# Performance work log

Measured on AMD Instinct MI355X. Metric: run time of the kernel, lower is better.

Reference implementation:

```python
import jax, jax.numpy as jnp
import numpy as np

NUM_HEADS = 16
EMBED_DIM = 1024
HEAD_DIM = EMBED_DIM // NUM_HEADS  # 64


def setup_inputs() -> dict:
    key = jax.random.key(0)
    k1, k2, k3 = jax.random.split(key, 3)
    x = jax.random.normal(k1, (2, 2048, EMBED_DIM), dtype=jnp.float32)
    # torch Linear(head_dim, 3*head_dim): weight [3*hd, hd], bias [3*hd]
    # stored here as W_qkv [hd, 3*hd] so that y = x @ W_qkv + b
    lim = 1.0 / np.sqrt(HEAD_DIM)
    W_qkv = jax.random.uniform(k2, (HEAD_DIM, 3 * HEAD_DIM), minval=-lim, maxval=lim, dtype=jnp.float32)
    b_qkv = jax.random.uniform(k3, (3 * HEAD_DIM,), minval=-lim, maxval=lim, dtype=jnp.float32)
    return {"x": x, "W_qkv": W_qkv, "b_qkv": b_qkv}


def reference(x, W_qkv, b_qkv):
    B, T, E = x.shape
    # [B, T, E] -> [B, H, T, hd]
    xh = x.reshape(B, T, NUM_HEADS, HEAD_DIM).transpose(0, 2, 1, 3)
    qkv = xh @ W_qkv + b_qkv  # [B, H, T, 3*hd], shared weights across heads
    q, k, v = jnp.split(qkv, 3, axis=-1)
    scale = 1.0 / jnp.sqrt(jnp.asarray(HEAD_DIM, dtype=x.dtype))
    scores = jnp.einsum('bhqd,bhkd->bhqk', q, k) * scale  # [B, H, T, T]
    attn = jax.nn.softmax(scores, axis=-1)
    out = jnp.einsum('bhqk,bhkd->bhqd', attn, v)  # [B, H, T, hd]
    return out.transpose(0, 2, 1, 3).reshape(B, T, E)
```

## Files before the change

kernel.cpp:

```cpp
#include <hip/hip_runtime.h>
#include <hip/hip_bf16.h>

#define T_SEQ   2048
#define EMBED   1024
#define HD      64
#define NHEADS  16
#define NBH     32
#define QSCALE  0.18033688011112042f

typedef __attribute__((ext_vector_type(8))) short short8;
typedef __attribute__((ext_vector_type(4))) float f32x4;
typedef __attribute__((ext_vector_type(2))) unsigned int uint2v;
typedef __attribute__((ext_vector_type(4))) unsigned int uint4v;

#if __has_builtin(__builtin_amdgcn_exp2f)
#define EXP2F __builtin_amdgcn_exp2f
#else
#define EXP2F exp2f
#endif

__device__ __forceinline__ ushort bf16r(float f) {
  union { float f; unsigned u; } v; v.f = f;
  return (ushort)((v.u + 0x8000u) >> 16);
}

__device__ __forceinline__ unsigned pk2bf_perm(float a, float b) {
  union { float f; unsigned u; } ua, ub; ua.f = a; ub.f = b;
  return __builtin_amdgcn_perm(ub.u + 0x8000u, ua.u + 0x8000u, 0x07060302u);
}
#if __has_builtin(__builtin_amdgcn_cvt_pk_bf16_f32)
typedef __attribute__((ext_vector_type(2))) __bf16 bf16x2;
__device__ __forceinline__ unsigned pkbf(float a, float b) {
  union { bf16x2 v; unsigned u; } c;
  c.v = __builtin_amdgcn_cvt_pk_bf16_f32(a, b);
  return c.u;
}
#else
#define pkbf pk2bf_perm
#endif

__device__ __forceinline__ uint2v pl32swap(unsigned a, unsigned b) {
#if __has_builtin(__builtin_amdgcn_permlane32_swap)
  return __builtin_amdgcn_permlane32_swap(a, b, false, false);
#else
  asm("v_permlane32_swap_b32 %0, %1" : "+v"(a), "+v"(b));
  return (uint2v){a, b};
#endif
}
__device__ __forceinline__ uint2v pl16swap(unsigned a, unsigned b) {
#if __has_builtin(__builtin_amdgcn_permlane16_swap)
  return __builtin_amdgcn_permlane16_swap(a, b, false, false);
#else
  asm("v_permlane16_swap_b32 %0, %1" : "+v"(a), "+v"(b));
  return (uint2v){a, b};
#endif
}

__device__ __forceinline__ void async16(const ushort* g, ushort* l) {
  __builtin_amdgcn_global_load_lds(
      (const __attribute__((address_space(1))) unsigned int*)g,
      (__attribute__((address_space(3))) unsigned int*)l, 16, 0, 0);
}

__global__ __launch_bounds__(256) void prep_w(const float* __restrict__ W,
                                              ushort* __restrict__ Wg) {
  const int i = blockIdx.x * 256 + threadIdx.x;
  const int d = i / 192, c = i - d * 192;
  const int phys = c * 64 + (((d >> 3) ^ (c & 7)) << 3) + (d & 7);
  Wg[phys] = bf16r(W[i]);
}

__global__ __launch_bounds__(256) void qkv_proj(
    const float* __restrict__ x, const ushort* __restrict__ Wg,
    const float* __restrict__ bias,
    ushort* __restrict__ Qws, ushort* __restrict__ Kws,
    ushort* __restrict__ Vtws) {
  __shared__ ushort WtL[192 * 64];
  __shared__ __attribute__((aligned(16))) float bl[192];

  const int bx = blockIdx.x;
  const int b  = bx >> 9;
  const int h  = (bx >> 5) & 15;
  const int t0 = (bx & 31) * 64;
  const int tid = threadIdx.x;
  const int wave = tid >> 6, lane = tid & 63;
  const int quad = lane >> 4, n16 = lane & 15;

  const int trow = t0 + wave * 16 + n16;
  const float* xr = x + ((size_t)(b * T_SEQ + trow)) * EMBED + h * HD;
  short8 xa[2];
#pragma unroll
  for (int ks = 0; ks < 2; ks++) {
    f32x4 v0 = *(const f32x4*)(xr + ks * 32 + quad * 8);
    f32x4 v1 = *(const f32x4*)(xr + ks * 32 + quad * 8 + 4);
    short8 f;
    ((unsigned*)&f)[0] = pkbf(v0[0], v0[1]);
    ((unsigned*)&f)[1] = pkbf(v0[2], v0[3]);
    ((unsigned*)&f)[2] = pkbf(v1[0], v1[1]);
    ((unsigned*)&f)[3] = pkbf(v1[2], v1[3]);
    xa[ks] = f;
  }

#pragma unroll
  for (int it = 0; it < 6; it++)
    async16(Wg + it * 2048 + tid * 8, WtL + it * 2048 + wave * 512);
  if (tid < 192) bl[tid] = bias[tid];
  __syncthreads();

  const int bh = b * NHEADS + h;
  const size_t qkbase = (size_t)bh * T_SEQ * HD;
  const int tw = t0 + wave * 16;
  const int sw = n16 & 7;
  const int t = tw + n16;

#pragma unroll
  for (int nt = 0; nt < 12; nt++) {
    const ushort* wrow = WtL + (nt * 16 + n16) * 64;
    const short8 wb0 = *(short8*)(wrow + ((quad ^ sw) << 3));
    const short8 wb1 = *(short8*)(wrow + (((4 | quad) ^ sw) << 3));
    if (nt < 8) {
      f32x4 acc = (f32x4){0.f, 0.f, 0.f, 0.f};
      acc = __builtin_amdgcn_mfma_f32_16x16x32_bf16(wb0, xa[0], acc, 0, 0, 0);
      acc = __builtin_amdgcn_mfma_f32_16x16x32_bf16(wb1, xa[1], acc, 0, 0, 0);
      const f32x4 bv4 = *(const f32x4*)(bl + nt * 16 + quad * 4);
      uint2v pk;
      if (nt < 4) {
        const int d = nt * 16 + quad * 4;
        pk.x = pkbf((acc[0] + bv4[0]) * QSCALE, (acc[1] + bv4[1]) * QSCALE);
        pk.y = pkbf((acc[2] + bv4[2]) * QSCALE, (acc[3] + bv4[3]) * QSCALE);
        *(uint2v*)(Qws + qkbase + (size_t)t * HD + d) = pk;
      } else {
        const int d = (nt - 4) * 16 + quad * 4;
        pk.x = pkbf(acc[0] + bv4[0], acc[1] + bv4[1]);
        pk.y = pkbf(acc[2] + bv4[2], acc[3] + bv4[3]);
        *(uint2v*)(Kws + qkbase + (size_t)t * HD + d) = pk;
      }
    } else {
      f32x4 acc = (f32x4){0.f, 0.f, 0.f, 0.f};
      acc = __builtin_amdgcn_mfma_f32_16x16x32_bf16(xa[0], wb0, acc, 0, 0, 0);
      acc = __builtin_amdgcn_mfma_f32_16x16x32_bf16(xa[1], wb1, acc, 0, 0, 0);
      const float bv = bl[nt * 16 + n16];
      const int d = (nt - 8) * 16 + n16;
      const int tcol = tw + quad * 4;
      uint2v pk;
      pk.x = pkbf(acc[0] + bv, acc[1] + bv);
      pk.y = pkbf(acc[2] + bv, acc[3] + bv);
      *(uint2v*)(Vtws + (size_t)(bh * HD + d) * T_SEQ + tcol) = pk;
    }
  }
}

__global__ __launch_bounds__(256) void flash_attn(
    const ushort* __restrict__ Qws, const ushort* __restrict__ Kws,
    const ushort* __restrict__ Vtws, float* __restrict__ out) {
  __shared__ ushort Ks[4][64 * 64];
  __shared__ ushort Vs[4][64 * 64];

  const int bx = blockIdx.x;
  const int bh = bx & 31;
  const int q0 = (bx >> 5) * 128;
  const int b = bh >> 4, h = bh & 15;
  const int tid = threadIdx.x;
  const int wave = tid >> 6, lane = tid & 63;
  const int quad = lane >> 4, n16 = lane & 15;

  const ushort* Qb = Qws + (size_t)bh * T_SEQ * HD;
  const ushort* Kb = Kws + (size_t)bh * T_SEQ * HD;
  const ushort* Vb = Vtws + (size_t)bh * HD * T_SEQ;

  short8 qa[2][2];
#pragma unroll
  for (int hf = 0; hf < 2; hf++)
#pragma unroll
    for (int ks = 0; ks < 2; ks++) {
      const int row = q0 + wave * 32 + hf * 16 + n16;
      qa[hf][ks] = *(const short8*)(Qb + (size_t)row * HD + ks * 32 + quad * 8);
    }

  const int sr = tid >> 3, sp = tid & 7;
  const int sl = (sp ^ (sr & 7)) * 8;
  const ushort* srcK0 = Kb + (size_t)sr * HD + sl;
  const ushort* srcK1 = Kb + (size_t)(sr + 32) * HD + sl;
  const ushort* srcV0 = Vb + (size_t)sr * T_SEQ + sl;
  const ushort* srcV1 = Vb + (size_t)(sr + 32) * T_SEQ + sl;

  int foff[2];
#pragma unroll
  for (int ks = 0; ks < 2; ks++)
    foff[ks] = n16 * 64 + ((((ks << 2) | quad) ^ (n16 & 7)) << 3);

  short8 ones;
#pragma unroll
  for (int j = 0; j < 8; j++) ones[j] = (short)0x3F80;

  f32x4 o[2][4];
  f32x4 lA[2];
#pragma unroll
  for (int hf = 0; hf < 2; hf++) {
    lA[hf] = (f32x4){0.f, 0.f, 0.f, 0.f};
#pragma unroll
    for (int nt = 0; nt < 4; nt++) o[hf][nt] = (f32x4){0.f, 0.f, 0.f, 0.f};
  }

  auto tile = [&](const ushort* Kt, const ushort* Vt) {
    f32x4 s0[4], s1[4];
    __builtin_amdgcn_s_setprio(1);
#pragma unroll
    for (int nt = 0; nt < 4; nt++) {
      const short8 ka0 = *(short8*)(Kt + (nt << 10) + foff[0]);
      const short8 ka1 = *(short8*)(Kt + (nt << 10) + foff[1]);
      f32x4 a0 = (f32x4){0.f, 0.f, 0.f, 0.f};
      f32x4 a1 = (f32x4){0.f, 0.f, 0.f, 0.f};
      a0 = __builtin_amdgcn_mfma_f32_16x16x32_bf16(ka0, qa[0][0], a0, 0, 0, 0);
      a0 = __builtin_amdgcn_mfma_f32_16x16x32_bf16(ka1, qa[0][1], a0, 0, 0, 0);
      a1 = __builtin_amdgcn_mfma_f32_16x16x32_bf16(ka0, qa[1][0], a1, 0, 0, 0);
      a1 = __builtin_amdgcn_mfma_f32_16x16x32_bf16(ka1, qa[1][1], a1, 0, 0, 0);
      s0[nt] = a0;
      s1[nt] = a1;
    }
    __builtin_amdgcn_s_setprio(0);

    short8 pa[2][2];
#pragma unroll
    for (int hf = 0; hf < 2; hf++) {
      unsigned P01[4], P23[4];
#pragma unroll
      for (int nt = 0; nt < 4; nt++) {
        const f32x4 sv = hf ? s1[nt] : s0[nt];
        float p0 = EXP2F(sv[0]), p1 = EXP2F(sv[1]);
        float p2 = EXP2F(sv[2]), p3 = EXP2F(sv[3]);
        P01[nt] = pkbf(p0, p1);
        P23[nt] = pkbf(p2, p3);
      }
#pragma unroll
      for (int ks = 0; ks < 2; ks++) {
        uint2v tA = pl32swap(P01[2 * ks], P01[2 * ks + 1]);
        uint2v uA = pl16swap(tA.x, tA.y);
        uint2v tB = pl32swap(P23[2 * ks], P23[2 * ks + 1]);
        uint2v uB = pl16swap(tB.x, tB.y);
        union { uint4v u; short8 s; } c;
        c.u = (uint4v){uA.x, uB.x, uA.y, uB.y};
        pa[hf][ks] = c.s;
      }
    }

    __builtin_amdgcn_s_setprio(1);
#pragma unroll
    for (int nt = 0; nt < 4; nt++) {
      const short8 vb0 = *(short8*)(Vt + (nt << 10) + foff[0]);
      const short8 vb1 = *(short8*)(Vt + (nt << 10) + foff[1]);
      o[0][nt] = __builtin_amdgcn_mfma_f32_16x16x32_bf16(pa[0][0], vb0, o[0][nt], 0, 0, 0);
      o[0][nt] = __builtin_amdgcn_mfma_f32_16x16x32_bf16(pa[0][1], vb1, o[0][nt], 0, 0, 0);
      o[1][nt] = __builtin_amdgcn_mfma_f32_16x16x32_bf16(pa[1][0], vb0, o[1][nt], 0, 0, 0);
      o[1][nt] = __builtin_amdgcn_mfma_f32_16x16x32_bf16(pa[1][1], vb1, o[1][nt], 0, 0, 0);
    }
#pragma unroll
    for (int hf = 0; hf < 2; hf++) {
      lA[hf] = __builtin_amdgcn_mfma_f32_16x16x32_bf16(pa[hf][0], ones, lA[hf], 0, 0, 0);
      lA[hf] = __builtin_amdgcn_mfma_f32_16x16x32_bf16(pa[hf][1], ones, lA[hf], 0, 0, 0);
    }
    __builtin_amdgcn_s_setprio(0);
  };

  async16(srcK0, Ks[0] + wave * 512);
  async16(srcK1, Ks[0] + 2048 + wave * 512);
  async16(srcV0, Vs[0] + wave * 512);
  async16(srcV1, Vs[0] + 2048 + wave * 512);
  async16(srcK0 + 64 * HD, Ks[1] + wave * 512);
  async16(srcK1 + 64 * HD, Ks[1] + 2048 + wave * 512);
  async16(srcV0 + 64, Vs[1] + wave * 512);
  async16(srcV1 + 64, Vs[1] + 2048 + wave * 512);
  srcK0 += 128 * HD; srcK1 += 128 * HD; srcV0 += 128; srcV1 += 128;

  for (int j = 0; j < 16; j++) {
    __builtin_amdgcn_sched_barrier(0);
    asm volatile("s_waitcnt vmcnt(0)" ::: "memory");
    __builtin_amdgcn_s_barrier();
    __builtin_amdgcn_sched_barrier(0);
    const int b0 = (j & 1) << 1;
    if (j < 15) {
      async16(srcK0, Ks[b0 ^ 2] + wave * 512);
      async16(srcK1, Ks[b0 ^ 2] + 2048 + wave * 512);
      async16(srcV0, Vs[b0 ^ 2] + wave * 512);
      async16(srcV1, Vs[b0 ^ 2] + 2048 + wave * 512);
      async16(srcK0 + 64 * HD, Ks[(b0 ^ 2) | 1] + wave * 512);
      async16(srcK1 + 64 * HD, Ks[(b0 ^ 2) | 1] + 2048 + wave * 512);
      async16(srcV0 + 64, Vs[(b0 ^ 2) | 1] + wave * 512);
      async16(srcV1 + 64, Vs[(b0 ^ 2) | 1] + 2048 + wave * 512);
      srcK0 += 128 * HD; srcK1 += 128 * HD; srcV0 += 128; srcV1 += 128;
    }
    tile(Ks[b0], Vs[b0]);
    tile(Ks[b0 | 1], Vs[b0 | 1]);
  }

#pragma unroll
  for (int hf = 0; hf < 2; hf++) {
#pragma unroll
    for (int r = 0; r < 4; r++) {
      const float rl = 1.0f / lA[hf][r];
      const int row = q0 + wave * 32 + hf * 16 + quad * 4 + r;
#pragma unroll
      for (int nt = 0; nt < 4; nt++) {
        const int d = nt * 16 + n16;
        out[(size_t)(b * T_SEQ + row) * EMBED + h * HD + d] = o[hf][nt][r] * rl;
      }
    }
  }
}

extern "C" void kernel_launch(void* const* d_in, const int* in_sizes, int n_in,
                              void* d_out, int out_size, void* d_ws, size_t ws_size,
                              hipStream_t stream) {
  (void)in_sizes; (void)n_in; (void)out_size; (void)ws_size;
  const float* x    = (const float*)d_in[0];
  const float* W    = (const float*)d_in[1];
  const float* bias = (const float*)d_in[2];
  float* out = (float*)d_out;

  const size_t elems = (size_t)NBH * T_SEQ * HD;
  ushort* Qws  = (ushort*)d_ws;
  ushort* Kws  = Qws + elems;
  ushort* Vtws = Kws + elems;
  ushort* Wg   = Vtws + elems;

  prep_w<<<dim3(48), dim3(256), 0, stream>>>(W, Wg);
  qkv_proj<<<dim3(1024), dim3(256), 0, stream>>>(x, Wg, bias, Qws, Kws, Vtws);
  flash_attn<<<dim3(512), dim3(256), 0, stream>>>(Qws, Kws, Vtws, out);
}
```

Before: 128.7 us.

## Fuse weight prep into projection and deepen K/V prefetch pipeline

Drops the separate prep_w kernel launch. Each projection block now loads the fp32 weights itself, converts them to bf16 and writes them into the swizzled LDS layout. The attention loop goes from paired 128-row tiles with a full vmcnt(0) drain to single 64-row tiles over a 4-slot ring. It prefetches two tiles ahead and uses partial vmcnt waits, so K/V loads overlap compute better. In exchange every projection block redoes the weight conversion, and the attention loop runs twice as many barriers.

```diff
diff --git a/kernel.cpp b/kernel.cpp
--- a/kernel.cpp
+++ b/kernel.cpp
@@ -62,16 +62,8 @@
       (__attribute__((address_space(3))) unsigned int*)l, 16, 0, 0);
 }
 
-__global__ __launch_bounds__(256) void prep_w(const float* __restrict__ W,
-                                              ushort* __restrict__ Wg) {
-  const int i = blockIdx.x * 256 + threadIdx.x;
-  const int d = i / 192, c = i - d * 192;
-  const int phys = c * 64 + (((d >> 3) ^ (c & 7)) << 3) + (d & 7);
-  Wg[phys] = bf16r(W[i]);
-}
-
 __global__ __launch_bounds__(256) void qkv_proj(
-    const float* __restrict__ x, const ushort* __restrict__ Wg,
+    const float* __restrict__ x, const float* __restrict__ W,
     const float* __restrict__ bias,
     ushort* __restrict__ Qws, ushort* __restrict__ Kws,
     ushort* __restrict__ Vtws) {
@@ -102,8 +94,18 @@
   }
 
 #pragma unroll
-  for (int it = 0; it < 6; it++)
-    async16(Wg + it * 2048 + tid * 8, WtL + it * 2048 + wave * 512);
+  for (int k = 0; k < 12; k++) {
+    const int i4 = k * 256 + tid;
+    const f32x4 w4 = *(const f32x4*)(W + (size_t)i4 * 4);
+    const int i = i4 * 4;
+    const int d = i / 192;
+    const int c0 = i - d * 192;
+#pragma unroll
+    for (int j = 0; j < 4; j++) {
+      const int c = c0 + j;
+      WtL[c * 64 + (((d >> 3) ^ (c & 7)) << 3) + (d & 7)] = bf16r(w4[j]);
+    }
+  }
   if (tid < 192) bl[tid] = bias[tid];
   __syncthreads();
 
@@ -179,10 +181,10 @@
 
   const int sr = tid >> 3, sp = tid & 7;
   const int sl = (sp ^ (sr & 7)) * 8;
-  const ushort* srcK0 = Kb + (size_t)sr * HD + sl;
-  const ushort* srcK1 = Kb + (size_t)(sr + 32) * HD + sl;
-  const ushort* srcV0 = Vb + (size_t)sr * T_SEQ + sl;
-  const ushort* srcV1 = Vb + (size_t)(sr + 32) * T_SEQ + sl;
+  const ushort* pK0 = Kb + (size_t)sr * HD + sl;
+  const ushort* pK1 = Kb + (size_t)(sr + 32) * HD + sl;
+  const ushort* pV0 = Vb + (size_t)sr * T_SEQ + sl;
+  const ushort* pV1 = Vb + (size_t)(sr + 32) * T_SEQ + sl;
 
   int foff[2];
 #pragma unroll
@@ -202,7 +204,36 @@
     for (int nt = 0; nt < 4; nt++) o[hf][nt] = (f32x4){0.f, 0.f, 0.f, 0.f};
   }
 
-  auto tile = [&](const ushort* Kt, const ushort* Vt) {
+  async16(pK0, Ks[0] + wave * 512);
+  async16(pK1, Ks[0] + 2048 + wave * 512);
+  async16(pV0, Vs[0] + wave * 512);
+  async16(pV1, Vs[0] + 2048 + wave * 512);
+  async16(pK0 + 64 * HD, Ks[1] + wave * 512);
+  async16(pK1 + 64 * HD, Ks[1] + 2048 + wave * 512);
+  async16(pV0 + 64, Vs[1] + wave * 512);
+  async16(pV1 + 64, Vs[1] + 2048 + wave * 512);
+  pK0 += 128 * HD; pK1 += 128 * HD; pV0 += 128; pV1 += 128;
+
+  for (int kt = 0; kt < 32; kt++) {
+    const int cb = kt & 3;
+    if (kt < 30) {
+      const int pb = (kt + 2) & 3;
+      async16(pK0, Ks[pb] + wave * 512);
+      async16(pK1, Ks[pb] + 2048 + wave * 512);
+      async16(pV0, Vs[pb] + wave * 512);
+      async16(pV1, Vs[pb] + 2048 + wave * 512);
+      pK0 += 64 * HD; pK1 += 64 * HD; pV0 += 64; pV1 += 64;
+    }
+    __builtin_amdgcn_sched_barrier(0);
+    if (kt < 30)       asm volatile("s_waitcnt vmcnt(8)" ::: "memory");
+    else if (kt == 30) asm volatile("s_waitcnt vmcnt(4)" ::: "memory");
+    else               asm volatile("s_waitcnt vmcnt(0)" ::: "memory");
+    __builtin_amdgcn_s_barrier();
+    __builtin_amdgcn_sched_barrier(0);
+
+    const ushort* Kt = Ks[cb];
+    const ushort* Vt = Vs[cb];
+
     f32x4 s0[4], s1[4];
     __builtin_amdgcn_s_setprio(1);
 #pragma unroll
@@ -260,37 +291,6 @@
       lA[hf] = __builtin_amdgcn_mfma_f32_16x16x32_bf16(pa[hf][1], ones, lA[hf], 0, 0, 0);
     }
     __builtin_amdgcn_s_setprio(0);
-  };
-
-  async16(srcK0, Ks[0] + wave * 512);
-  async16(srcK1, Ks[0] + 2048 + wave * 512);
-  async16(srcV0, Vs[0] + wave * 512);
-  async16(srcV1, Vs[0] + 2048 + wave * 512);
-  async16(srcK0 + 64 * HD, Ks[1] + wave * 512);
-  async16(srcK1 + 64 * HD, Ks[1] + 2048 + wave * 512);
-  async16(srcV0 + 64, Vs[1] + wave * 512);
-  async16(srcV1 + 64, Vs[1] + 2048 + wave * 512);
-  srcK0 += 128 * HD; srcK1 += 128 * HD; srcV0 += 128; srcV1 += 128;
-
-  for (int j = 0; j < 16; j++) {
-    __builtin_amdgcn_sched_barrier(0);
-    asm volatile("s_waitcnt vmcnt(0)" ::: "memory");
-    __builtin_amdgcn_s_barrier();
-    __builtin_amdgcn_sched_barrier(0);
-    const int b0 = (j & 1) << 1;
-    if (j < 15) {
-      async16(srcK0, Ks[b0 ^ 2] + wave * 512);
-      async16(srcK1, Ks[b0 ^ 2] + 2048 + wave * 512);
-      async16(srcV0, Vs[b0 ^ 2] + wave * 512);
-      async16(srcV1, Vs[b0 ^ 2] + 2048 + wave * 512);
-      async16(srcK0 + 64 * HD, Ks[(b0 ^ 2) | 1] + wave * 512);
-      async16(srcK1 + 64 * HD, Ks[(b0 ^ 2) | 1] + 2048 + wave * 512);
-      async16(srcV0 + 64, Vs[(b0 ^ 2) | 1] + wave * 512);
-      async16(srcV1 + 64, Vs[(b0 ^ 2) | 1] + 2048 + wave * 512);
-      srcK0 += 128 * HD; srcK1 += 128 * HD; srcV0 += 128; srcV1 += 128;
-    }
-    tile(Ks[b0], Vs[b0]);
-    tile(Ks[b0 | 1], Vs[b0 | 1]);
   }
 
 #pragma unroll
@@ -321,9 +321,7 @@
   ushort* Qws  = (ushort*)d_ws;
   ushort* Kws  = Qws + elems;
   ushort* Vtws = Kws + elems;
-  ushort* Wg   = Vtws + elems;
-
-  prep_w<<<dim3(48), dim3(256), 0, stream>>>(W, Wg);
-  qkv_proj<<<dim3(1024), dim3(256), 0, stream>>>(x, Wg, bias, Qws, Kws, Vtws);
+
+  qkv_proj<<<dim3(1024), dim3(256), 0, stream>>>(x, W, bias, Qws, Kws, Vtws);
   flash_attn<<<dim3(512), dim3(256), 0, stream>>>(Qws, Kws, Vtws, out);
 }
```

New measurement: 128.2 us. About the same (-0.3%).

## Use two waves per attention block with 64 query rows each and deeper K/V pipeline

Applied to the files above, without the earlier changes.

The flash attention kernel now runs 128 threads per block, with each wave handling 64 query rows (four 16-row groups) instead of 32. Each K/V tile loaded from LDS is reused across more queries. The K/V staging becomes a four-slot ring with prefetch two tiles ahead and partial vmcnt waits, replacing the wait-for-all double buffer. The trade is more accumulator registers per wave and fewer waves per block, which may lower occupancy.

```diff
diff --git a/kernel.cpp b/kernel.cpp
--- a/kernel.cpp
+++ b/kernel.cpp
@@ -150,7 +150,7 @@
   }
 }
 
-__global__ __launch_bounds__(256) void flash_attn(
+__global__ __launch_bounds__(128) void flash_attn(
     const ushort* __restrict__ Qws, const ushort* __restrict__ Kws,
     const ushort* __restrict__ Vtws, float* __restrict__ out) {
   __shared__ ushort Ks[4][64 * 64];
@@ -168,21 +168,19 @@
   const ushort* Kb = Kws + (size_t)bh * T_SEQ * HD;
   const ushort* Vb = Vtws + (size_t)bh * HD * T_SEQ;
 
-  short8 qa[2][2];
-#pragma unroll
-  for (int hf = 0; hf < 2; hf++)
+  short8 qa[4][2];
+#pragma unroll
+  for (int qg = 0; qg < 4; qg++)
 #pragma unroll
     for (int ks = 0; ks < 2; ks++) {
-      const int row = q0 + wave * 32 + hf * 16 + n16;
-      qa[hf][ks] = *(const short8*)(Qb + (size_t)row * HD + ks * 32 + quad * 8);
-    }
-
-  const int sr = tid >> 3, sp = tid & 7;
-  const int sl = (sp ^ (sr & 7)) * 8;
-  const ushort* srcK0 = Kb + (size_t)sr * HD + sl;
-  const ushort* srcK1 = Kb + (size_t)(sr + 32) * HD + sl;
-  const ushort* srcV0 = Vb + (size_t)sr * T_SEQ + sl;
-  const ushort* srcV1 = Vb + (size_t)(sr + 32) * T_SEQ + sl;
+      const int row = q0 + wave * 64 + qg * 16 + n16;
+      qa[qg][ks] = *(const short8*)(Qb + (size_t)row * HD + ks * 32 + quad * 8);
+    }
+
+  const int sr8 = lane >> 3, sp = lane & 7;
+  const int sl = (sp ^ sr8) * 8;
+  const ushort* pK = Kb + (size_t)(wave * 32 + sr8) * HD + sl;
+  const ushort* pV = Vb + (size_t)(wave * 32 + sr8) * T_SEQ + sl;
 
   int foff[2];
 #pragma unroll
@@ -193,42 +191,73 @@
 #pragma unroll
   for (int j = 0; j < 8; j++) ones[j] = (short)0x3F80;
 
-  f32x4 o[2][4];
-  f32x4 lA[2];
-#pragma unroll
-  for (int hf = 0; hf < 2; hf++) {
-    lA[hf] = (f32x4){0.f, 0.f, 0.f, 0.f};
-#pragma unroll
-    for (int nt = 0; nt < 4; nt++) o[hf][nt] = (f32x4){0.f, 0.f, 0.f, 0.f};
-  }
-
-  auto tile = [&](const ushort* Kt, const ushort* Vt) {
-    f32x4 s0[4], s1[4];
-    __builtin_amdgcn_s_setprio(1);
+  f32x4 o[4][4];
+  f32x4 lA[4];
+#pragma unroll
+  for (int qg = 0; qg < 4; qg++) {
+    lA[qg] = (f32x4){0.f, 0.f, 0.f, 0.f};
+#pragma unroll
+    for (int nt = 0; nt < 4; nt++) o[qg][nt] = (f32x4){0.f, 0.f, 0.f, 0.f};
+  }
+
+#pragma unroll
+  for (int j = 0; j < 4; j++) {
+    async16(pK + j * 8 * HD, Ks[0] + wave * 2048 + j * 512);
+    async16(pV + j * 8 * T_SEQ, Vs[0] + wave * 2048 + j * 512);
+  }
+#pragma unroll
+  for (int j = 0; j < 4; j++) {
+    async16(pK + 64 * HD + j * 8 * HD, Ks[1] + wave * 2048 + j * 512);
+    async16(pV + 64 + j * 8 * T_SEQ, Vs[1] + wave * 2048 + j * 512);
+  }
+  pK += 128 * HD; pV += 128;
+
+  for (int kt = 0; kt < 32; kt++) {
+    const int cb = kt & 3;
+    if (kt < 30) {
+      const int pb = (kt + 2) & 3;
+#pragma unroll
+      for (int j = 0; j < 4; j++) {
+        async16(pK + j * 8 * HD, Ks[pb] + wave * 2048 + j * 512);
+        async16(pV + j * 8 * T_SEQ, Vs[pb] + wave * 2048 + j * 512);
+      }
+      pK += 64 * HD; pV += 64;
+    }
+    __builtin_amdgcn_sched_barrier(0);
+    if (kt < 30)       asm volatile("s_waitcnt vmcnt(16)" ::: "memory");
+    else if (kt == 30) asm volatile("s_waitcnt vmcnt(8)" ::: "memory");
+    else               asm volatile("s_waitcnt vmcnt(0)" ::: "memory");
+    __builtin_amdgcn_s_barrier();
+    __builtin_amdgcn_sched_barrier(0);
+
+    const ushort* Kt = Ks[cb];
+    const ushort* Vt = Vs[cb];
+
+    short8 ka[4][2];
 #pragma unroll
     for (int nt = 0; nt < 4; nt++) {
-      const short8 ka0 = *(short8*)(Kt + (nt << 10) + foff[0]);
-      const short8 ka1 = *(short8*)(Kt + (nt << 10) + foff[1]);
-      f32x4 a0 = (f32x4){0.f, 0.f, 0.f, 0.f};
-      f32x4 a1 = (f32x4){0.f, 0.f, 0.f, 0.f};
-      a0 = __builtin_amdgcn_mfma_f32_16x16x32_bf16(ka0, qa[0][0], a0, 0, 0, 0);
-      a0 = __builtin_amdgcn_mfma_f32_16x16x32_bf16(ka1, qa[0][1], a0, 0, 0, 0);
-      a1 = __builtin_amdgcn_mfma_f32_16x16x32_bf16(ka0, qa[1][0], a1, 0, 0, 0);
-      a1 = __builtin_amdgcn_mfma_f32_16x16x32_bf16(ka1, qa[1][1], a1, 0, 0, 0);
-      s0[nt] = a0;
-      s1[nt] = a1;
-    }
-    __builtin_amdgcn_s_setprio(0);
-
-    short8 pa[2][2];
-#pragma unroll
-    for (int hf = 0; hf < 2; hf++) {
+      ka[nt][0] = *(short8*)(Kt + (nt << 10) + foff[0]);
+      ka[nt][1] = *(short8*)(Kt + (nt << 10) + foff[1]);
+    }
+
+    short8 pa[4][2];
+#pragma unroll
+    for (int qg = 0; qg < 4; qg++) {
+      f32x4 s[4];
+      __builtin_amdgcn_s_setprio(1);
+#pragma unroll
+      for (int nt = 0; nt < 4; nt++) {
+        f32x4 a = (f32x4){0.f, 0.f, 0.f, 0.f};
+        a = __builtin_amdgcn_mfma_f32_16x16x32_bf16(ka[nt][0], qa[qg][0], a, 0, 0, 0);
+        a = __builtin_amdgcn_mfma_f32_16x16x32_bf16(ka[nt][1], qa[qg][1], a, 0, 0, 0);
+        s[nt] = a;
+      }
+      __builtin_amdgcn_s_setprio(0);
       unsigned P01[4], P23[4];
 #pragma unroll
       for (int nt = 0; nt < 4; nt++) {
-        const f32x4 sv = hf ? s1[nt] : s0[nt];
-        float p0 = EXP2F(sv[0]), p1 = EXP2F(sv[1]);
-        float p2 = EXP2F(sv[2]), p3 = EXP2F(sv[3]);
+        float p0 = EXP2F(s[nt][0]), p1 = EXP2F(s[nt][1]);
+        float p2 = EXP2F(s[nt][2]), p3 = EXP2F(s[nt][3]);
         P01[nt] = pkbf(p0, p1);
         P23[nt] = pkbf(p2, p3);
       }
@@ -240,69 +269,39 @@
         uint2v uB = pl16swap(tB.x, tB.y);
         union { uint4v u; short8 s; } c;
         c.u = (uint4v){uA.x, uB.x, uA.y, uB.y};
-        pa[hf][ks] = c.s;
+        pa[qg][ks] = c.s;
       }
     }
 
     __builtin_amdgcn_s_setprio(1);
+#pragma unroll
+    for (int qg = 0; qg < 4; qg++) {
+      lA[qg] = __builtin_amdgcn_mfma_f32_16x16x32_bf16(pa[qg][0], ones, lA[qg], 0, 0, 0);
+      lA[qg] = __builtin_amdgcn_mfma_f32_16x16x32_bf16(pa[qg][1], ones, lA[qg], 0, 0, 0);
+    }
 #pragma unroll
     for (int nt = 0; nt < 4; nt++) {
       const short8 vb0 = *(short8*)(Vt + (nt << 10) + foff[0]);
       const short8 vb1 = *(short8*)(Vt + (nt << 10) + foff[1]);
-      o[0][nt] = __builtin_amdgcn_mfma_f32_16x16x32_bf16(pa[0][0], vb0, o[0][nt], 0, 0, 0);
-      o[0][nt] = __builtin_amdgcn_mfma_f32_16x16x32_bf16(pa[0][1], vb1, o[0][nt], 0, 0, 0);
-      o[1][nt] = __builtin_amdgcn_mfma_f32_16x16x32_bf16(pa[1][0], vb0, o[1][nt], 0, 0, 0);
-      o[1][nt] = __builtin_amdgcn_mfma_f32_16x16x32_bf16(pa[1][1], vb1, o[1][nt], 0, 0, 0);
-    }
-#pragma unroll
-    for (int hf = 0; hf < 2; hf++) {
-      lA[hf] = __builtin_amdgcn_mfma_f32_16x16x32_bf16(pa[hf][0], ones, lA[hf], 0, 0, 0);
-      lA[hf] = __builtin_amdgcn_mfma_f32_16x16x32_bf16(pa[hf][1], ones, lA[hf], 0, 0, 0);
+#pragma unroll
+      for (int qg = 0; qg < 4; qg++) {
+        o[qg][nt] = __builtin_amdgcn_mfma_f32_16x16x32_bf16(pa[qg][0], vb0, o[qg][nt], 0, 0, 0);
+        o[qg][nt] = __builtin_amdgcn_mfma_f32_16x16x32_bf16(pa[qg][1], vb1, o[qg][nt], 0, 0, 0);
+      }
     }
     __builtin_amdgcn_s_setprio(0);
-  };
-
-  async16(srcK0, Ks[0] + wave * 512);
-  async16(srcK1, Ks[0] + 2048 + wave * 512);
-  async16(srcV0, Vs[0] + wave * 512);
-  async16(srcV1, Vs[0] + 2048 + wave * 512);
-  async16(srcK0 + 64 * HD, Ks[1] + wave * 512);
-  async16(srcK1 + 64 * HD, Ks[1] + 2048 + wave * 512);
-  async16(srcV0 + 64, Vs[1] + wave * 512);
-  async16(srcV1 + 64, Vs[1] + 2048 + wave * 512);
-  srcK0 += 128 * HD; srcK1 += 128 * HD; srcV0 += 128; srcV1 += 128;
-
-  for (int j = 0; j < 16; j++) {
-    __builtin_amdgcn_sched_barrier(0);
-    asm volatile("s_waitcnt vmcnt(0)" ::: "memory");
-    __builtin_amdgcn_s_barrier();
-    __builtin_amdgcn_sched_barrier(0);
-    const int b0 = (j & 1) << 1;
-    if (j < 15) {
-      async16(srcK0, Ks[b0 ^ 2] + wave * 512);
-      async16(srcK1, Ks[b0 ^ 2] + 2048 + wave * 512);
-      async16(srcV0, Vs[b0 ^ 2] + wave * 512);
-      async16(srcV1, Vs[b0 ^ 2] + 2048 + wave * 512);
-      async16(srcK0 + 64 * HD, Ks[(b0 ^ 2) | 1] + wave * 512);
-      async16(srcK1 + 64 * HD, Ks[(b0 ^ 2) | 1] + 2048 + wave * 512);
-      async16(srcV0 + 64, Vs[(b0 ^ 2) | 1] + wave * 512);
-      async16(srcV1 + 64, Vs[(b0 ^ 2) | 1] + 2048 + wave * 512);
-      srcK0 += 128 * HD; srcK1 += 128 * HD; srcV0 += 128; srcV1 += 128;
-    }
-    tile(Ks[b0], Vs[b0]);
-    tile(Ks[b0 | 1], Vs[b0 | 1]);
-  }
-
-#pragma unroll
-  for (int hf = 0; hf < 2; hf++) {
+  }
+
+#pragma unroll
+  for (int qg = 0; qg < 4; qg++) {
 #pragma unroll
     for (int r = 0; r < 4; r++) {
-      const float rl = 1.0f / lA[hf][r];
-      const int row = q0 + wave * 32 + hf * 16 + quad * 4 + r;
+      const float rl = 1.0f / lA[qg][r];
+      const int row = q0 + wave * 64 + qg * 16 + quad * 4 + r;
 #pragma unroll
       for (int nt = 0; nt < 4; nt++) {
         const int d = nt * 16 + n16;
-        out[(size_t)(b * T_SEQ + row) * EMBED + h * HD + d] = o[hf][nt][r] * rl;
+        out[(size_t)(b * T_SEQ + row) * EMBED + h * HD + d] = o[qg][nt][r] * rl;
       }
     }
   }
@@ -325,5 +324,5 @@
 
   prep_w<<<dim3(48), dim3(256), 0, stream>>>(W, Wg);
   qkv_proj<<<dim3(1024), dim3(256), 0, stream>>>(x, Wg, bias, Qws, Kws, Vtws);
-  flash_attn<<<dim3(512), dim3(256), 0, stream>>>(Qws, Kws, Vtws, out);
-}
+  flash_attn<<<dim3(512), dim3(128), 0, stream>>>(Qws, Kws, Vtws, out);
+}
```

Result: slower. 139.9 us (+8.7%).
